# Kernel tuning notes

Measured on AMD Instinct MI355X. Metric: run time of the kernel, lower is better.

## Reference

```python
import jax, jax.numpy as jnp
import numpy as np

ALPHA = 0.2  # LeakyReLU negative slope


def setup_inputs() -> dict:
    key = jax.random.key(0)
    k_h, k_adj, k_a1, k_a2 = jax.random.split(key, 4)
    B, N, D = 8, 2048, 128
    h = jax.random.normal(k_h, (B, N, D), dtype=jnp.float32)
    adj = jax.random.randint(k_adj, (B, N, N), 0, 2, dtype=jnp.int32)
    # attention parameters a1, a2: shape (D, 1) as in the original layer
    a1 = jax.random.normal(k_a1, (D, 1), dtype=jnp.float32) * (1.0 / np.sqrt(D))
    a2 = jax.random.normal(k_a2, (D, 1), dtype=jnp.float32) * (1.0 / np.sqrt(D))
    return {"h": h, "adj": adj, "a1": a1, "a2": a2}


def reference(h, adj, a1, a2):
    # h: [B, N, D]; adj: [B, N, N] (int mask); a1, a2: [D, 1]
    f1 = h @ a1                                  # [B, N, 1] per-source score
    f2 = h @ a2                                  # [B, N, 1] per-target score
    logits = f1 + jnp.swapaxes(f2, 1, 2)         # broadcast -> [B, N, N]
    logits = jnp.where(logits > 0, logits, ALPHA * logits)  # LeakyReLU
    logits = jnp.where(adj > 0, logits, -jnp.inf)            # adjacency mask
    prob = jax.nn.softmax(logits, axis=2)        # [B, N, N]
    h_prime = jnp.einsum('bij,bjd->bid', prob, h)  # weighted aggregation
    return jax.nn.elu(h_prime)                   # concat=True branch
```

## Files before the change

kernel.cpp:

```cpp
#include <hip/hip_runtime.h>
#include <hip/hip_bf16.h>
#include <math.h>

#define BB 8
#define NN 2048
#define DD 128
#define ALPHA 0.2f
#define LOG2E 1.4426950408889634f

typedef __attribute__((ext_vector_type(8))) short short8;
typedef __attribute__((ext_vector_type(4))) float f32x4;

__device__ inline unsigned short bf16_rne(float v) {
    unsigned int x = __float_as_uint(v);
    unsigned int r = x + 0x7FFFu + ((x >> 16) & 1u);
    return (unsigned short)(r >> 16);
}
__device__ inline float bf16_back(unsigned short u) {
    return __uint_as_float(((unsigned int)u) << 16);
}

__global__ __launch_bounds__(256) void pack_kernel(const float* __restrict__ h,
                                                   const float* __restrict__ a1,
                                                   const float* __restrict__ a2,
                                                   float* __restrict__ f1,
                                                   float* __restrict__ f2,
                                                   unsigned short* __restrict__ panel) {
    __shared__ float hs[32][DD];
    int blk = blockIdx.x;
    int b   = blk >> 6;
    int ks  = blk & 63;
    int r0  = ks * 32;
    int t   = threadIdx.x;

    const float* hb = h + ((size_t)b * NN + r0) * DD;
#pragma unroll
    for (int m = 0; m < 4; ++m) {
        int off = t * 4 + m * 1024;
        *reinterpret_cast<float4*>(&hs[0][0] + off) =
            *reinterpret_cast<const float4*>(hb + off);
    }
    __syncthreads();

    {
        int row = t >> 3, d0 = (t & 7) * 16;
        float s1 = 0.f, s2 = 0.f;
#pragma unroll
        for (int q = 0; q < 4; ++q) {
            float4 hv  = *reinterpret_cast<const float4*>(&hs[row][d0 + q * 4]);
            float4 av1 = *reinterpret_cast<const float4*>(a1 + d0 + q * 4);
            float4 av2 = *reinterpret_cast<const float4*>(a2 + d0 + q * 4);
            s1 += hv.x * av1.x + hv.y * av1.y + hv.z * av1.z + hv.w * av1.w;
            s2 += hv.x * av2.x + hv.y * av2.y + hv.z * av2.z + hv.w * av2.w;
        }
#pragma unroll
        for (int off = 1; off < 8; off <<= 1) {
            s1 += __shfl_xor(s1, off, 64);
            s2 += __shfl_xor(s2, off, 64);
        }
        if ((t & 7) == 0) {
            f1[b * NN + r0 + row] = s1 * LOG2E;
            f2[b * NN + r0 + row] = s2 * LOG2E;
        }
    }

    {
        int n = t >> 1;
        size_t base = (((size_t)b * 64 + ks) * 128 + n) * 32;
#pragma unroll
        for (int cc = 0; cc < 2; ++cc) {
            int c = (t & 1) * 2 + cc;
            short8 v;
#pragma unroll
            for (int e = 0; e < 8; ++e) v[e] = (short)bf16_rne(hs[c * 8 + e][n]);
            *reinterpret_cast<short8*>(panel + base + (size_t)c * 8) = v;
        }
    }
}

__global__ __launch_bounds__(256, 4) void gat_mfma(const int* __restrict__ adj,
                                                   const float* __restrict__ f1,
                                                   const float* __restrict__ f2,
                                                   const unsigned short* __restrict__ panel,
                                                   float* __restrict__ out) {
    __shared__ float buf[2][16][132];
    __shared__ float sden[4][16];

    int blk  = blockIdx.x;
    int b    = blk & 7;
    int tile = blk >> 3;
    int i0   = tile * 16;
    int t    = threadIdx.x;
    int w    = t >> 6, l = t & 63;
    int lr   = l & 15, lc = l >> 4;

    const unsigned short* pb = panel + (size_t)b * (64 * 128 * 32);
    const float* f2b = f2 + b * NN;
    const int* arow  = adj + (size_t)b * NN * NN + (size_t)(i0 + lr) * NN;
    float f1r = f1[b * NN + i0 + lr];

    f32x4 acc[8];
#pragma unroll
    for (int nt = 0; nt < 8; ++nt) acc[nt] = (f32x4){0.f, 0.f, 0.f, 0.f};
    float sacc = 0.f;

    int kbase = w * 512;

    int jb0 = kbase + lc * 8;
    int4   ajN0 = *reinterpret_cast<const int4*>(arow + jb0);
    int4   ajN1 = *reinterpret_cast<const int4*>(arow + jb0 + 4);
    float4 f2N0 = *reinterpret_cast<const float4*>(f2b + jb0);
    float4 f2N1 = *reinterpret_cast<const float4*>(f2b + jb0 + 4);

#pragma unroll
    for (int ks = 0; ks < 16; ++ks) {
        int k0 = kbase + ks * 32;
        int4 a0 = ajN0, a1 = ajN1;
        float4 g0 = f2N0, g1 = f2N1;

        const unsigned short* pk = pb + (size_t)(k0 >> 5) * 4096 + lr * 32 + lc * 8;
        short8 bf[8];
#pragma unroll
        for (int nt = 0; nt < 8; ++nt)
            bf[nt] = *reinterpret_cast<const short8*>(pk + nt * 512);

        if (ks < 15) {
            int jn = k0 + 32 + lc * 8;
            ajN0 = *reinterpret_cast<const int4*>(arow + jn);
            ajN1 = *reinterpret_cast<const int4*>(arow + jn + 4);
            f2N0 = *reinterpret_cast<const float4*>(f2b + jn);
            f2N1 = *reinterpret_cast<const float4*>(f2b + jn + 4);
        }

        float f2v[8] = {g0.x, g0.y, g0.z, g0.w, g1.x, g1.y, g1.z, g1.w};
        int   aj[8]  = {a0.x, a0.y, a0.z, a0.w, a1.x, a1.y, a1.z, a1.w};

        short8 af;
#pragma unroll
        for (int e = 0; e < 8; ++e) {
            float x  = f1r + f2v[e];
            float ee = fmaxf(x, ALPHA * x);
            float wv = (aj[e] > 0) ? __builtin_amdgcn_exp2f(ee) : 0.f;
            unsigned short u = bf16_rne(wv);
            sacc += bf16_back(u);
            af[e] = (short)u;
        }
#pragma unroll
        for (int nt = 0; nt < 8; ++nt)
            acc[nt] = __builtin_amdgcn_mfma_f32_16x16x32_bf16(af, bf[nt], acc[nt], 0, 0, 0);
    }

    sacc += __shfl_xor(sacc, 16, 64);
    sacc += __shfl_xor(sacc, 32, 64);
    if (l < 16) sden[w][l] = sacc;

    float* mybuf = &buf[w >> 1][0][0];
    if ((w & 1) == 0) {
#pragma unroll
        for (int nt = 0; nt < 8; ++nt) {
            float* p = mybuf + (lc * 4) * 132 + nt * 16 + lr;
#pragma unroll
            for (int r = 0; r < 4; ++r) p[r * 132] = acc[nt][r];
        }
    }
    __syncthreads();
    if (w & 1) {
#pragma unroll
        for (int nt = 0; nt < 8; ++nt) {
            float* p = mybuf + (lc * 4) * 132 + nt * 16 + lr;
#pragma unroll
            for (int r = 0; r < 4; ++r) p[r * 132] += acc[nt][r];
        }
    }
    __syncthreads();

    {
        int row = t >> 4, col0 = (t & 15) * 8;
        float den = sden[0][row] + sden[1][row] + sden[2][row] + sden[3][row];
        float inv = 1.0f / den;
        float* ob = out + ((size_t)b * NN + i0 + row) * DD;
#pragma unroll
        for (int q = 0; q < 2; ++q) {
            int col = col0 + q * 4;
            float4 v0 = *reinterpret_cast<const float4*>(&buf[0][row][col]);
            float4 v1 = *reinterpret_cast<const float4*>(&buf[1][row][col]);
            float r0 = (v0.x + v1.x) * inv;
            float r1 = (v0.y + v1.y) * inv;
            float r2 = (v0.z + v1.z) * inv;
            float r3 = (v0.w + v1.w) * inv;
            r0 = (r0 > 0.f) ? r0 : expm1f(r0);
            r1 = (r1 > 0.f) ? r1 : expm1f(r1);
            r2 = (r2 > 0.f) ? r2 : expm1f(r2);
            r3 = (r3 > 0.f) ? r3 : expm1f(r3);
            *reinterpret_cast<float4*>(ob + col) = make_float4(r0, r1, r2, r3);
        }
    }
}

extern "C" void kernel_launch(void* const* d_in, const int* in_sizes, int n_in,
                              void* d_out, int out_size, void* d_ws, size_t ws_size,
                              hipStream_t stream) {
    const float* h   = (const float*)d_in[0];
    const int*   adj = (const int*)d_in[1];
    const float* a1  = (const float*)d_in[2];
    const float* a2  = (const float*)d_in[3];
    float* out = (float*)d_out;

    float* f1 = (float*)d_ws;
    float* f2 = f1 + BB * NN;
    unsigned short* panel = (unsigned short*)(f2 + BB * NN);

    pack_kernel<<<BB * 64, 256, 0, stream>>>(h, a1, a2, f1, f2, panel);
    gat_mfma<<<BB * 128, 256, 0, stream>>>(adj, f1, f2, panel, out);
}
```

Before: 243.5 us.

## Bit-pack adjacency mask in separate kernel and compute denominator via MFMA

Adds a pre-pass kernel that compresses the int32 adjacency matrix into one bit per entry. The main attention kernel then reads the packed bits instead of full int rows. The softmax denominator is now an extra MFMA against a ones vector rather than a per-lane scalar sum plus shuffles, and the bf16 conversion uses the packed intrinsic. The main kernel's adjacency traffic shrinks, but the full int mask must still be read once by the new kernel, and the f2 prefetch double-buffering was dropped.

```diff
diff --git a/kernel.cpp b/kernel.cpp
--- a/kernel.cpp
+++ b/kernel.cpp
@@ -16,8 +16,27 @@
     unsigned int r = x + 0x7FFFu + ((x >> 16) & 1u);
     return (unsigned short)(r >> 16);
 }
-__device__ inline float bf16_back(unsigned short u) {
-    return __uint_as_float(((unsigned int)u) << 16);
+
+__global__ __launch_bounds__(256) void bitpack_kernel(const int* __restrict__ adj,
+                                                      unsigned* __restrict__ bits) {
+    unsigned g0 = blockIdx.x * 256 + threadIdx.x;
+#pragma unroll
+    for (int rep = 0; rep < 2; ++rep) {
+        unsigned g = g0 + rep * 524288u;
+        const int4* p = reinterpret_cast<const int4*>(adj + (size_t)g * 32);
+        int4 v[8];
+#pragma unroll
+        for (int i = 0; i < 8; ++i) v[i] = p[i];
+        unsigned w = 0;
+#pragma unroll
+        for (int i = 0; i < 8; ++i) {
+            w |= ((unsigned)v[i].x) << (4 * i);
+            w |= ((unsigned)v[i].y) << (4 * i + 1);
+            w |= ((unsigned)v[i].z) << (4 * i + 2);
+            w |= ((unsigned)v[i].w) << (4 * i + 3);
+        }
+        bits[g] = w;
+    }
 }
 
 __global__ __launch_bounds__(256) void pack_kernel(const float* __restrict__ h,
@@ -78,7 +97,7 @@
     }
 }
 
-__global__ __launch_bounds__(256, 4) void gat_mfma(const int* __restrict__ adj,
+__global__ __launch_bounds__(256, 4) void gat_mfma(const unsigned* __restrict__ bits,
                                                    const float* __restrict__ f1,
                                                    const float* __restrict__ f2,
                                                    const unsigned short* __restrict__ panel,
@@ -96,27 +115,31 @@
 
     const unsigned short* pb = panel + (size_t)b * (64 * 128 * 32);
     const float* f2b = f2 + b * NN;
-    const int* arow  = adj + (size_t)b * NN * NN + (size_t)(i0 + lr) * NN;
     float f1r = f1[b * NN + i0 + lr];
 
+    int kbase = w * 512;
+    const unsigned* brow = bits + (((size_t)(b * NN + i0 + lr)) << 6) + (kbase >> 5);
+
     f32x4 acc[8];
 #pragma unroll
     for (int nt = 0; nt < 8; ++nt) acc[nt] = (f32x4){0.f, 0.f, 0.f, 0.f};
-    float sacc = 0.f;
-
-    int kbase = w * 512;
-
-    int jb0 = kbase + lc * 8;
-    int4   ajN0 = *reinterpret_cast<const int4*>(arow + jb0);
-    int4   ajN1 = *reinterpret_cast<const int4*>(arow + jb0 + 4);
-    float4 f2N0 = *reinterpret_cast<const float4*>(f2b + jb0);
-    float4 f2N1 = *reinterpret_cast<const float4*>(f2b + jb0 + 4);
+    f32x4 accd = (f32x4){0.f, 0.f, 0.f, 0.f};
+
+    short8 ones;
+#pragma unroll
+    for (int e = 0; e < 8; ++e) ones[e] = (short)0x3F80;
+
+    unsigned bcur = brow[0];
 
 #pragma unroll
     for (int ks = 0; ks < 16; ++ks) {
         int k0 = kbase + ks * 32;
-        int4 a0 = ajN0, a1 = ajN1;
-        float4 g0 = f2N0, g1 = f2N1;
+        int jb = k0 + lc * 8;
+        unsigned bs = bcur >> (lc * 8);
+        if (ks < 15) bcur = brow[ks + 1];
+
+        float4 g0 = *reinterpret_cast<const float4*>(f2b + jb);
+        float4 g1 = *reinterpret_cast<const float4*>(f2b + jb + 4);
 
         const unsigned short* pk = pb + (size_t)(k0 >> 5) * 4096 + lr * 32 + lc * 8;
         short8 bf[8];
@@ -124,35 +147,30 @@
         for (int nt = 0; nt < 8; ++nt)
             bf[nt] = *reinterpret_cast<const short8*>(pk + nt * 512);
 
-        if (ks < 15) {
-            int jn = k0 + 32 + lc * 8;
-            ajN0 = *reinterpret_cast<const int4*>(arow + jn);
-            ajN1 = *reinterpret_cast<const int4*>(arow + jn + 4);
-            f2N0 = *reinterpret_cast<const float4*>(f2b + jn);
-            f2N1 = *reinterpret_cast<const float4*>(f2b + jn + 4);
-        }
-
         float f2v[8] = {g0.x, g0.y, g0.z, g0.w, g1.x, g1.y, g1.z, g1.w};
-        int   aj[8]  = {a0.x, a0.y, a0.z, a0.w, a1.x, a1.y, a1.z, a1.w};
-
-        short8 af;
+        float wv[8];
 #pragma unroll
         for (int e = 0; e < 8; ++e) {
             float x  = f1r + f2v[e];
             float ee = fmaxf(x, ALPHA * x);
-            float wv = (aj[e] > 0) ? __builtin_amdgcn_exp2f(ee) : 0.f;
-            unsigned short u = bf16_rne(wv);
-            sacc += bf16_back(u);
-            af[e] = (short)u;
-        }
+            float gv = __builtin_amdgcn_exp2f(ee);
+            wv[e] = ((bs >> e) & 1u) ? gv : 0.f;
+        }
+        union { short8 s; __hip_bfloat162 h2[4]; } u;
+#pragma unroll
+        for (int p = 0; p < 4; ++p)
+            u.h2[p] = __float22bfloat162_rn(make_float2(wv[2 * p], wv[2 * p + 1]));
+
 #pragma unroll
         for (int nt = 0; nt < 8; ++nt)
-            acc[nt] = __builtin_amdgcn_mfma_f32_16x16x32_bf16(af, bf[nt], acc[nt], 0, 0, 0);
-    }
-
-    sacc += __shfl_xor(sacc, 16, 64);
-    sacc += __shfl_xor(sacc, 32, 64);
-    if (l < 16) sden[w][l] = sacc;
+            acc[nt] = __builtin_amdgcn_mfma_f32_16x16x32_bf16(u.s, bf[nt], acc[nt], 0, 0, 0);
+        accd = __builtin_amdgcn_mfma_f32_16x16x32_bf16(u.s, ones, accd, 0, 0, 0);
+    }
+
+    if ((l & 15) == 0) {
+#pragma unroll
+        for (int r = 0; r < 4; ++r) sden[w][(l >> 4) * 4 + r] = accd[r];
+    }
 
     float* mybuf = &buf[w >> 1][0][0];
     if ((w & 1) == 0) {
@@ -209,7 +227,9 @@
     float* f1 = (float*)d_ws;
     float* f2 = f1 + BB * NN;
     unsigned short* panel = (unsigned short*)(f2 + BB * NN);
-
+    unsigned* bits = (unsigned*)(panel + (size_t)BB * 64 * 128 * 32);
+
+    bitpack_kernel<<<2048, 256, 0, stream>>>(adj, bits);
     pack_kernel<<<BB * 64, 256, 0, stream>>>(h, a1, a2, f1, f2, panel);
-    gat_mfma<<<BB * 128, 256, 0, stream>>>(adj, f1, f2, panel, out);
-}
+    gat_mfma<<<BB * 128, 256, 0, stream>>>(bits, f1, f2, panel, out);
+}
```

Result: no change. 244.8 us (+0.5%).
